# Performance work log

Hardware: AMD Instinct MI355X
Metric: run time of the kernel (lower is better)

The kernel has to match this reference:

```python
import jax, jax.numpy as jnp
import numpy as np

B, N, DOP, DM, H = 8, 2048, 256, 256, 256  # batch, n_ops==n_machines, dims


def setup_inputs() -> dict:
    key = jax.random.key(0)
    ks = jax.random.split(key, 21)
    s = 0.02
    inp = {
        "operation_features": jax.random.normal(ks[0], (B, N, DOP), jnp.float32),
        "machine_features": jax.random.normal(ks[1], (B, N, DM), jnp.float32),
        "type_match_mask": jax.random.bernoulli(ks[2], 0.3, (B, N, N)).astype(jnp.float32),
        "same_type_mask": jax.random.bernoulli(ks[3], 0.3, (B, N, N)).astype(jnp.float32),
        "oma_q_w": jax.random.normal(ks[4], (H, DM), jnp.float32) * s,
        "oma_q_b": jnp.zeros((H,), jnp.float32),
        "oma_kv_w": jax.random.normal(ks[5], (2 * H, DOP), jnp.float32) * s,
        "oma_kv_b": jnp.zeros((2 * H,), jnp.float32),
        "oma_s_w": jax.random.normal(ks[6], (1, 2 * H), jnp.float32) * s,
        "oma_s_b": jnp.zeros((1,), jnp.float32),
        "oma_o_w": jax.random.normal(ks[7], (DM, H), jnp.float32) * s,
        "oma_o_b": jnp.zeros((DM,), jnp.float32),
        "sa_w_w": jax.random.normal(ks[8], (3 * H, DM), jnp.float32) * s,
        "sa_w_b": jnp.zeros((3 * H,), jnp.float32),
        "sa_s_w": jax.random.normal(ks[9], (1, 2 * H), jnp.float32) * s,
        "sa_s_b": jnp.zeros((1,), jnp.float32),
        "sa_o_w": jax.random.normal(ks[10], (DM, H), jnp.float32) * s,
        "sa_o_b": jnp.zeros((DM,), jnp.float32),
        "mix_w": jax.random.normal(ks[11], (DM, 2 * DM), jnp.float32) * s,
        "mix_b": jnp.zeros((DM,), jnp.float32),
    }
    return inp


def reference(operation_features, machine_features, type_match_mask, same_type_mask,
              oma_q_w, oma_q_b, oma_kv_w, oma_kv_b, oma_s_w, oma_s_b, oma_o_w, oma_o_b,
              sa_w_w, sa_w_b, sa_s_w, sa_s_b, sa_o_w, sa_o_b, mix_w, mix_b):
    # --- OperationMachineAttention ---
    q = machine_features @ oma_q_w.T + oma_q_b            # (B,M,H)
    kv = operation_features @ oma_kv_w.T + oma_kv_b       # (B,C,2H)
    k, v = jnp.split(kv, 2, axis=-1)
    # Linear(cat([q,k])) == q @ W[:, :H].T + k @ W[:, H:].T + b (additive-score factorization)
    sq = jnp.einsum('bmh,h->bm', q, oma_s_w[0, :H])
    sk = jnp.einsum('bch,h->bc', k, oma_s_w[0, H:])
    scores = jax.nn.leaky_relu(sq[:, :, None] + sk[:, None, :] + oma_s_b[0])  # (B,M,C)
    p = jax.nn.softmax(scores * type_match_mask, axis=-1)
    wf = jnp.einsum('bmc,bch->bmh', p, v)
    operation_machine = wf @ oma_o_w.T + oma_o_b           # (B,M,DM)

    # --- SelfAttention over machines ---
    w3 = machine_features @ sa_w_w.T + sa_w_b              # (B,C,3H)
    q2, k2, v2 = jnp.split(w3, 3, axis=-1)
    sq2 = jnp.einsum('bih,h->bi', q2, sa_s_w[0, :H])
    sk2 = jnp.einsum('bjh,h->bj', k2, sa_s_w[0, H:])
    s2 = jax.nn.leaky_relu(sq2[:, :, None] + sk2[:, None, :] + sa_s_b[0])  # (B,C,C)
    p2 = jax.nn.softmax(s2 * same_type_mask, axis=-1)
    machine_machine = jnp.einsum('bij,bjh->bih', p2, v2) @ sa_o_w.T + sa_o_b  # (B,C,DM)

    # --- mix ---
    mixed = jnp.concatenate([operation_machine, machine_machine], axis=-1)
    return mixed @ mix_w.T + mix_b                          # (B,N,DM)
```

## Files before the change

### kernel.cpp

```cpp
#include <hip/hip_runtime.h>
#include <stdint.h>
#include <stddef.h>

#define B_ 8
#define N_ 2048
#define C_ 2048
#define D_ 256
#define H_ 256

typedef __bf16 bf16x8 __attribute__((ext_vector_type(8)));
typedef __bf16 bf16x4 __attribute__((ext_vector_type(4)));
typedef float f32x4 __attribute__((ext_vector_type(4)));

#define MFMA16(a, b, c) __builtin_amdgcn_mfma_f32_16x16x32_bf16((a), (b), (c), 0, 0, 0)

__global__ __launch_bounds__(256) void k0a_partial(
    const float* __restrict__ oma_q_w, const float* __restrict__ oma_kv_w,
    const float* __restrict__ sa_w_w,
    const float* __restrict__ oma_s_w, const float* __restrict__ sa_s_w,
    float* __restrict__ partial)
{
    int d = threadIdx.x;
    int vec = blockIdx.x >> 3, hc = blockIdx.x & 7;
    int h0 = hc * 32;
    const float* Wb; const float* sv;
    if (vec == 0)      { Wb = oma_q_w  + h0 * 256;         sv = oma_s_w + h0; }
    else if (vec == 1) { Wb = oma_kv_w + h0 * 256;         sv = oma_s_w + 256 + h0; }
    else if (vec == 2) { Wb = sa_w_w   + h0 * 256;         sv = sa_s_w + h0; }
    else               { Wb = sa_w_w   + (256 + h0) * 256; sv = sa_s_w + 256 + h0; }
    float a = 0.f;
    #pragma unroll 8
    for (int h = 0; h < 32; ++h) a += Wb[h * 256 + d] * sv[h];
    partial[blockIdx.x * 256 + d] = a;
}

__global__ __launch_bounds__(256) void k0b_reduce(
    const float* __restrict__ partial,
    const float* __restrict__ oma_q_b, const float* __restrict__ oma_kv_b,
    const float* __restrict__ oma_s_w, const float* __restrict__ oma_s_b,
    const float* __restrict__ sa_w_b, const float* __restrict__ sa_s_w,
    const float* __restrict__ sa_s_b,
    float* __restrict__ wq_v, float* __restrict__ wk_v,
    float* __restrict__ wq2_v, float* __restrict__ wk2_v,
    float* __restrict__ sb)
{
    int d = threadIdx.x;
    float a0 = 0.f, a1 = 0.f, a2 = 0.f, a3 = 0.f;
    #pragma unroll
    for (int hc = 0; hc < 8; ++hc) {
        a0 += partial[(0 * 8 + hc) * 256 + d];
        a1 += partial[(1 * 8 + hc) * 256 + d];
        a2 += partial[(2 * 8 + hc) * 256 + d];
        a3 += partial[(3 * 8 + hc) * 256 + d];
    }
    wq_v[d] = a0; wk_v[d] = a1; wq2_v[d] = a2; wk2_v[d] = a3;

    int h = d;
    float p1 = oma_q_b[h] * oma_s_w[h] + oma_kv_b[h] * oma_s_w[256 + h];
    float p2 = sa_w_b[h] * sa_s_w[h] + sa_w_b[256 + h] * sa_s_w[256 + h];
    for (int o = 32; o; o >>= 1) { p1 += __shfl_xor(p1, o); p2 += __shfl_xor(p2, o); }
    __shared__ float redA[4], redB[4];
    int wv = threadIdx.x >> 6;
    if ((threadIdx.x & 63) == 0) { redA[wv] = p1; redB[wv] = p2; }
    __syncthreads();
    if (threadIdx.x == 0) {
        sb[0] = redA[0] + redA[1] + redA[2] + redA[3] + oma_s_b[0];
        sb[1] = redB[0] + redB[1] + redB[2] + redB[3] + sa_s_b[0];
    }
}

__global__ __launch_bounds__(256) void k1_wcat(
    const float* __restrict__ mix_w, const float* __restrict__ mix_b,
    const float* __restrict__ oma_o_w, const float* __restrict__ oma_o_b,
    const float* __restrict__ sa_o_w, const float* __restrict__ sa_o_b,
    __bf16* __restrict__ Wcat, float* __restrict__ b_total)
{
    int d = blockIdx.x, h = threadIdx.x;
    const float* mwr = mix_w + d * 512;
    float w1 = 0.f, w2 = 0.f;
    for (int e = 0; e < 256; ++e) {
        w1 += mwr[e] * oma_o_w[e * 256 + h];
        w2 += mwr[256 + e] * sa_o_w[e * 256 + h];
    }
    Wcat[d * 512 + h] = (__bf16)w1;
    Wcat[d * 512 + 256 + h] = (__bf16)w2;

    float pb = mwr[h] * oma_o_b[h] + mwr[256 + h] * sa_o_b[h];
    for (int o = 32; o; o >>= 1) pb += __shfl_xor(pb, o);
    __shared__ float red[4];
    if ((h & 63) == 0) red[h >> 6] = pb;
    __syncthreads();
    if (h == 0) b_total[d] = mix_b[d] + red[0] + red[1] + red[2] + red[3];
}

__global__ __launch_bounds__(256) void k2_scores(
    const float* __restrict__ op, const float* __restrict__ mach,
    const float* __restrict__ wq_v, const float* __restrict__ wk_v,
    const float* __restrict__ wq2_v, const float* __restrict__ wk2_v,
    const float* __restrict__ sb,
    float* __restrict__ sqp, float* __restrict__ skv,
    float* __restrict__ sq2p, float* __restrict__ sk2v)
{
    int t = threadIdx.x, lane = t & 63, wv = t >> 6;
    size_t n = (size_t)blockIdx.x * 4 + wv;
    const float4 mf = *(const float4*)(mach + n * 256 + lane * 4);
    const float4 of = *(const float4*)(op + n * 256 + lane * 4);
    const float4 q4 = *(const float4*)(wq_v + lane * 4);
    const float4 k4 = *(const float4*)(wk_v + lane * 4);
    const float4 q24 = *(const float4*)(wq2_v + lane * 4);
    const float4 k24 = *(const float4*)(wk2_v + lane * 4);
    float s1 = mf.x * q4.x + mf.y * q4.y + mf.z * q4.z + mf.w * q4.w;
    float s2 = of.x * k4.x + of.y * k4.y + of.z * k4.z + of.w * k4.w;
    float s3 = mf.x * q24.x + mf.y * q24.y + mf.z * q24.z + mf.w * q24.w;
    float s4 = mf.x * k24.x + mf.y * k24.y + mf.z * k24.z + mf.w * k24.w;
    for (int o = 32; o; o >>= 1) {
        s1 += __shfl_xor(s1, o); s2 += __shfl_xor(s2, o);
        s3 += __shfl_xor(s3, o); s4 += __shfl_xor(s4, o);
    }
    if (lane == 0) {
        sqp[n] = s1 + sb[0]; skv[n] = s2;
        sq2p[n] = s3 + sb[1]; sk2v[n] = s4;
    }
}

__global__ __launch_bounds__(256, 2) void k3_vgemm(
    const float* __restrict__ op, const float* __restrict__ mach,
    const float* __restrict__ oma_kv_w, const float* __restrict__ sa_w_w,
    __bf16* __restrict__ vt)
{
    __shared__ __attribute__((aligned(16))) __bf16 As[64][72];
    __shared__ __attribute__((aligned(16))) __bf16 Bs[64][72];
    int t = threadIdx.x;
    int bid = blockIdx.x;
    int which = bid >> 10;
    int r = bid & 1023;
    int b = r >> 7;
    int ht = (r >> 5) & 3;
    int ct = r & 31;

    const float* Aglob = (which ? (sa_w_w + 512 * 256) : (oma_kv_w + 256 * 256)) + ht * 64 * 256;
    const float* Bglob = (which ? mach : op) + ((size_t)b * N_ + ct * 64) * 256;

    int lane = t & 63, wv = t >> 6;
    int l15 = lane & 15, qo = (lane >> 4) * 8;
    int rr = t >> 4;
    int dd = (t & 15) * 4;

    f32x4 acc[4] = {};

    for (int d0 = 0; d0 < 256; d0 += 64) {
        #pragma unroll
        for (int p = 0; p < 4; ++p) {
            float4 av = *(const float4*)(Aglob + (size_t)(p * 16 + rr) * 256 + d0 + dd);
            float4 bv = *(const float4*)(Bglob + (size_t)(p * 16 + rr) * 256 + d0 + dd);
            bf16x4 a4, b4;
            a4[0] = (__bf16)av.x; a4[1] = (__bf16)av.y; a4[2] = (__bf16)av.z; a4[3] = (__bf16)av.w;
            b4[0] = (__bf16)bv.x; b4[1] = (__bf16)bv.y; b4[2] = (__bf16)bv.z; b4[3] = (__bf16)bv.w;
            *(bf16x4*)&As[p * 16 + rr][dd] = a4;
            *(bf16x4*)&Bs[p * 16 + rr][dd] = b4;
        }
        __syncthreads();
        #pragma unroll
        for (int kb = 0; kb < 2; ++kb) {
            bf16x8 bfr = *(const bf16x8*)&Bs[16 * wv + l15][kb * 32 + qo];
            #pragma unroll
            for (int rt = 0; rt < 4; ++rt) {
                bf16x8 afr = *(const bf16x8*)&As[16 * rt + l15][kb * 32 + qo];
                acc[rt] = MFMA16(afr, bfr, acc[rt]);
            }
        }
        __syncthreads();
    }
    #pragma unroll
    for (int rt = 0; rt < 4; ++rt)
        #pragma unroll
        for (int j = 0; j < 4; ++j)
            As[16 * rt + (lane >> 4) * 4 + j][16 * wv + l15] = (__bf16)acc[rt][j];
    __syncthreads();
    int hh = t >> 2, cb = (t & 3) * 16;
    __bf16* orow = vt + (((size_t)(which * 8 + b)) * 256 + ht * 64 + hh) * 2048 + ct * 64 + cb;
    *(bf16x8*)(orow) = *(const bf16x8*)&As[hh][cb];
    *(bf16x8*)(orow + 8) = *(const bf16x8*)&As[hh][cb + 8];
}

__device__ __forceinline__ f32x4 ntload4f(const float* p) {
    return __builtin_nontemporal_load(reinterpret_cast<const f32x4*>(p));
}

__global__ __launch_bounds__(256, 4) void k4_attn(
    const float* __restrict__ tmask, const float* __restrict__ smask,
    const float* __restrict__ sqp, const float* __restrict__ skv,
    const float* __restrict__ sq2p, const float* __restrict__ sk2v,
    const __bf16* __restrict__ vt,
    __bf16* __restrict__ wfcat)
{
    __shared__ __attribute__((aligned(16))) __bf16 smem[32 * 264];
    __shared__ float rowsum[32];
    __bf16* eA0 = smem;
    __bf16* eA1 = smem + 32 * 72;

    int t = threadIdx.x;
    int bid = blockIdx.x;
    int wg = (bid & 7) * 128 + (bid >> 3);
    int which = wg >> 9;
    int r = wg & 511;
    int b = r >> 6;
    int m0 = (r & 63) * 32;

    const float* mask = (which ? smask : tmask) + ((size_t)b * N_ + m0) * C_;
    const float* sqrow = (which ? sq2p : sqp) + b * N_ + m0;
    const float* skrow = (which ? sk2v : skv) + b * N_;
    const __bf16* vbase = vt + ((size_t)(which * 8 + b)) * 256 * 2048;

    int lane = t & 63, wv = t >> 6;
    int l15 = lane & 15, qo = (lane >> 4) * 8;
    int mrow = t >> 3;
    int cq8 = (t & 7) * 8;

    const __bf16* vptr = vbase + (size_t)(64 * wv + l15) * 2048 + qo;
    const float* mrowp = mask + (size_t)mrow * C_ + cq8;

    float sqv = sqrow[mrow];
    float psum = 0.f;
    f32x4 acc[2][4] = {};

    bf16x8 bfr[4][2];
    float mkA[8], skA[8], mkB[8], skB[8];

    auto load_ms = [&](int c0, float* mk, float* sk) {
        f32x4 a = ntload4f(mrowp + c0);
        f32x4 bq = ntload4f(mrowp + c0 + 4);
        f32x4 s0 = *(const f32x4*)(skrow + c0 + cq8);
        f32x4 s1 = *(const f32x4*)(skrow + c0 + cq8 + 4);
        #pragma unroll
        for (int i = 0; i < 4; ++i) {
            mk[i] = a[i]; mk[4 + i] = bq[i];
            sk[i] = s0[i]; sk[4 + i] = s1[i];
        }
    };
    auto load_bfr = [&](int c0) {
        #pragma unroll
        for (int ct = 0; ct < 4; ++ct)
            #pragma unroll
            for (int kb = 0; kb < 2; ++kb)
                bfr[ct][kb] = *(const bf16x8*)(vptr + (size_t)ct * 16 * 2048 + c0 + kb * 32);
    };
    auto compute_e = [&](const float* mk, const float* sk, __bf16* eb) {
        bf16x8 ev;
        #pragma unroll
        for (int i = 0; i < 8; ++i) {
            float s = sqv + sk[i];
            s = s > 0.f ? s : 0.01f * s;
            float e = __expf(s * mk[i]);
            psum += e;
            ev[i] = (__bf16)e;
        }
        *(bf16x8*)&eb[mrow * 72 + cq8] = ev;
    };
    auto do_mfma = [&](const __bf16* eb) {
        #pragma unroll
        for (int kb = 0; kb < 2; ++kb) {
            bf16x8 afr0 = *(const bf16x8*)&eb[l15 * 72 + kb * 32 + qo];
            bf16x8 afr1 = *(const bf16x8*)&eb[(16 + l15) * 72 + kb * 32 + qo];
            #pragma unroll
            for (int ct = 0; ct < 4; ++ct) {
                acc[0][ct] = MFMA16(afr0, bfr[ct][kb], acc[0][ct]);
                acc[1][ct] = MFMA16(afr1, bfr[ct][kb], acc[1][ct]);
            }
        }
    };

    load_ms(0, mkA, skA);
    load_ms(64, mkB, skB);
    load_bfr(0);

    #pragma unroll 1
    for (int c0 = 0; c0 < C_; c0 += 128) {
        compute_e(mkA, skA, eA0);
        int cA = c0 + 128; if (cA >= C_) cA = 0;
        load_ms(cA, mkA, skA);
        asm volatile("s_waitcnt lgkmcnt(0)" ::: "memory");
        __builtin_amdgcn_s_barrier();
        do_mfma(eA0);
        load_bfr(c0 + 64);
        compute_e(mkB, skB, eA1);
        int cB = c0 + 192; if (cB >= C_) cB = 0;
        load_ms(cB, mkB, skB);
        asm volatile("s_waitcnt lgkmcnt(0)" ::: "memory");
        __builtin_amdgcn_s_barrier();
        do_mfma(eA1);
        int cN = c0 + 128; if (cN >= C_) cN = 0;
        load_bfr(cN);
    }

    float rs = psum;
    rs += __shfl_xor(rs, 1);
    rs += __shfl_xor(rs, 2);
    rs += __shfl_xor(rs, 4);
    if ((t & 7) == 0) rowsum[mrow] = rs;
    __syncthreads();

    __bf16* obuf = smem;
    #pragma unroll
    for (int rt = 0; rt < 2; ++rt) {
        #pragma unroll
        for (int j = 0; j < 4; ++j) {
            int m = 16 * rt + (lane >> 4) * 4 + j;
            float inv = __builtin_amdgcn_rcpf(rowsum[m]);
            #pragma unroll
            for (int ct = 0; ct < 4; ++ct)
                obuf[m * 264 + 64 * wv + 16 * ct + l15] = (__bf16)(acc[rt][ct][j] * inv);
        }
    }
    __syncthreads();
    int m = t >> 3, cb = (t & 7) * 32;
    __bf16* wrow = wfcat + ((size_t)(b * N_ + m0 + m)) * 512 + which * 256 + cb;
    #pragma unroll
    for (int k = 0; k < 4; ++k)
        *(bf16x8*)(wrow + k * 8) = *(const bf16x8*)&obuf[m * 264 + cb + k * 8];
}

__global__ __launch_bounds__(256, 2) void k5_out(
    const __bf16* __restrict__ wfcat, const __bf16* __restrict__ Wcat,
    const float* __restrict__ b_total, float* __restrict__ out)
{
    __shared__ __attribute__((aligned(16))) __bf16 As[32][72];
    __shared__ __attribute__((aligned(16))) __bf16 Bs[256][72];
    __shared__ float bias[256];
    int t = threadIdx.x;
    int n0 = blockIdx.x * 32;
    int lane = t & 63, wv = t >> 6, l15 = lane & 15, qo = (lane >> 4) * 8;
    bias[t] = b_total[t];
    int ar = t >> 3;
    int ac = (t & 7) * 8;
    f32x4 acc[2][4] = {};

    for (int k0 = 0; k0 < 512; k0 += 64) {
        *(bf16x8*)&As[ar][ac] =
            *(const bf16x8*)(wfcat + (size_t)(n0 + ar) * 512 + k0 + ac);
        #pragma unroll
        for (int p = 0; p < 8; ++p)
            *(bf16x8*)&Bs[p * 32 + ar][ac] =
                *(const bf16x8*)(Wcat + (size_t)(p * 32 + ar) * 512 + k0 + ac);
        __syncthreads();
        #pragma unroll
        for (int kb = 0; kb < 2; ++kb) {
            bf16x8 afr[2];
            #pragma unroll
            for (int rt = 0; rt < 2; ++rt)
                afr[rt] = *(const bf16x8*)&As[16 * rt + l15][kb * 32 + qo];
            #pragma unroll
            for (int ct = 0; ct < 4; ++ct) {
                bf16x8 bfr = *(const bf16x8*)&Bs[64 * wv + 16 * ct + l15][kb * 32 + qo];
                #pragma unroll
                for (int rt = 0; rt < 2; ++rt)
                    acc[rt][ct] = MFMA16(afr[rt], bfr, acc[rt][ct]);
            }
        }
        __syncthreads();
    }
    #pragma unroll
    for (int rt = 0; rt < 2; ++rt) {
        #pragma unroll
        for (int ct = 0; ct < 4; ++ct) {
            int d = 64 * wv + 16 * ct + l15;
            float bv = bias[d];
            #pragma unroll
            for (int j = 0; j < 4; ++j) {
                int m = 16 * rt + (lane >> 4) * 4 + j;
                out[(size_t)(n0 + m) * 256 + d] = acc[rt][ct][j] + bv;
            }
        }
    }
}

extern "C" void kernel_launch(void* const* d_in, const int* in_sizes, int n_in,
                              void* d_out, int out_size, void* d_ws, size_t ws_size,
                              hipStream_t stream)
{
    const float* op_feat  = (const float*)d_in[0];
    const float* mach_feat= (const float*)d_in[1];
    const float* tmask    = (const float*)d_in[2];
    const float* smask    = (const float*)d_in[3];
    const float* oma_q_w  = (const float*)d_in[4];
    const float* oma_q_b  = (const float*)d_in[5];
    const float* oma_kv_w = (const float*)d_in[6];
    const float* oma_kv_b = (const float*)d_in[7];
    const float* oma_s_w  = (const float*)d_in[8];
    const float* oma_s_b  = (const float*)d_in[9];
    const float* oma_o_w  = (const float*)d_in[10];
    const float* oma_o_b  = (const float*)d_in[11];
    const float* sa_w_w   = (const float*)d_in[12];
    const float* sa_w_b   = (const float*)d_in[13];
    const float* sa_s_w   = (const float*)d_in[14];
    const float* sa_s_b   = (const float*)d_in[15];
    const float* sa_o_w   = (const float*)d_in[16];
    const float* sa_o_b   = (const float*)d_in[17];
    const float* mix_w    = (const float*)d_in[18];
    const float* mix_b    = (const float*)d_in[19];

    char* ws = (char*)d_ws;
    float* wq_v   = (float*)(ws + 0);
    float* wk_v   = (float*)(ws + 1024);
    float* wq2_v  = (float*)(ws + 2048);
    float* wk2_v  = (float*)(ws + 3072);
    float* sb     = (float*)(ws + 4096);
    float* btot   = (float*)(ws + 4352);
    float* sqp    = (float*)(ws + 8192);
    float* skv    = (float*)(ws + 73728);
    float* sq2p   = (float*)(ws + 139264);
    float* sk2v   = (float*)(ws + 204800);
    __bf16* Wcat  = (__bf16*)(ws + 270336);
    __bf16* vt    = (__bf16*)(ws + 532480);
    __bf16* wfcat = (__bf16*)(ws + 17309696);
    float* outp   = (float*)d_out;

    float* partial = (float*)(ws + 532480);

    k0a_partial<<<32, 256, 0, stream>>>(oma_q_w, oma_kv_w, sa_w_w,
                                        oma_s_w, sa_s_w, partial);
    k0b_reduce<<<1, 256, 0, stream>>>(partial, oma_q_b, oma_kv_b, oma_s_w, oma_s_b,
                                      sa_w_b, sa_s_w, sa_s_b,
                                      wq_v, wk_v, wq2_v, wk2_v, sb);
    k1_wcat<<<256, 256, 0, stream>>>(mix_w, mix_b, oma_o_w, oma_o_b,
                                     sa_o_w, sa_o_b, Wcat, btot);
    k2_scores<<<4096, 256, 0, stream>>>(op_feat, mach_feat, wq_v, wk_v, wq2_v, wk2_v,
                                        sb, sqp, skv, sq2p, sk2v);
    k3_vgemm<<<2048, 256, 0, stream>>>(op_feat, mach_feat, oma_kv_w, sa_w_w, vt);
    k4_attn<<<1024, 256, 0, stream>>>(tmask, smask, sqp, skv, sq2p, sk2v, vt, wfcat);
    k5_out<<<512, 256, 0, stream>>>(wfcat, Wcat, btot, outp);
}
```

Before: 475.5 us.

## Double k4_attn row tile to 64 rows and double-buffer V fragments

Each attention workgroup now handles 64 query rows instead of 32, so every V fragment loaded from global memory feeds four row tiles of MFMAs instead of two. This halves V traffic per output row, and the grid shrinks from 1024 to 512 blocks. V fragments are now double-buffered in registers (vA/vB) and prefetched alongside the mask and score loads. The cost is a larger accumulator and register footprint, with launch bounds lowered to 2 waves per SIMD, so occupancy and latency hiding drop and there are fewer blocks to spread across CUs.

Result: faster. 450.0 us (-5.4%).

```diff
diff --git a/kernel.cpp b/kernel.cpp
--- a/kernel.cpp
+++ b/kernel.cpp
@@ -187,25 +187,25 @@
     return __builtin_nontemporal_load(reinterpret_cast<const f32x4*>(p));
 }
 
-__global__ __launch_bounds__(256, 4) void k4_attn(
+__global__ __launch_bounds__(256, 2) void k4_attn(
     const float* __restrict__ tmask, const float* __restrict__ smask,
     const float* __restrict__ sqp, const float* __restrict__ skv,
     const float* __restrict__ sq2p, const float* __restrict__ sk2v,
     const __bf16* __restrict__ vt,
     __bf16* __restrict__ wfcat)
 {
-    __shared__ __attribute__((aligned(16))) __bf16 smem[32 * 264];
-    __shared__ float rowsum[32];
+    __shared__ __attribute__((aligned(16))) __bf16 smem[64 * 264];
+    __shared__ float rowsum[64];
     __bf16* eA0 = smem;
-    __bf16* eA1 = smem + 32 * 72;
+    __bf16* eA1 = smem + 64 * 72;
 
     int t = threadIdx.x;
     int bid = blockIdx.x;
-    int wg = (bid & 7) * 128 + (bid >> 3);
-    int which = wg >> 9;
-    int r = wg & 511;
-    int b = r >> 6;
-    int m0 = (r & 63) * 32;
+    int wg = (bid & 7) * 64 + (bid >> 3);
+    int which = wg >> 8;
+    int r = wg & 255;
+    int b = r >> 5;
+    int m0 = (r & 31) * 64;
 
     const float* mask = (which ? smask : tmask) + ((size_t)b * N_ + m0) * C_;
     const float* sqrow = (which ? sq2p : sqp) + b * N_ + m0;
@@ -214,95 +214,95 @@
 
     int lane = t & 63, wv = t >> 6;
     int l15 = lane & 15, qo = (lane >> 4) * 8;
-    int mrow = t >> 3;
-    int cq8 = (t & 7) * 8;
+    int mrow = t >> 2;
+    int cq16 = (t & 3) * 16;
 
     const __bf16* vptr = vbase + (size_t)(64 * wv + l15) * 2048 + qo;
-    const float* mrowp = mask + (size_t)mrow * C_ + cq8;
+    const float* mrowp = mask + (size_t)mrow * C_ + cq16;
+    const float* skp = skrow + cq16;
 
     float sqv = sqrow[mrow];
     float psum = 0.f;
-    f32x4 acc[2][4] = {};
-
-    bf16x8 bfr[4][2];
-    float mkA[8], skA[8], mkB[8], skB[8];
-
-    auto load_ms = [&](int c0, float* mk, float* sk) {
-        f32x4 a = ntload4f(mrowp + c0);
-        f32x4 bq = ntload4f(mrowp + c0 + 4);
-        f32x4 s0 = *(const f32x4*)(skrow + c0 + cq8);
-        f32x4 s1 = *(const f32x4*)(skrow + c0 + cq8 + 4);
-        #pragma unroll
-        for (int i = 0; i < 4; ++i) {
-            mk[i] = a[i]; mk[4 + i] = bq[i];
-            sk[i] = s0[i]; sk[4 + i] = s1[i];
-        }
+    f32x4 acc[4][4] = {};
+
+    bf16x8 vA[8], vB[8];
+    f32x4 mkA[4], mkB[4], skA[4], skB[4];
+
+    auto load_v = [&](bf16x8* v, int c0) {
+        #pragma unroll
+        for (int ct = 0; ct < 4; ++ct)
+            #pragma unroll
+            for (int kb = 0; kb < 2; ++kb)
+                v[ct * 2 + kb] = *(const bf16x8*)(vptr + (size_t)ct * 16 * 2048 + c0 + kb * 32);
     };
-    auto load_bfr = [&](int c0) {
-        #pragma unroll
-        for (int ct = 0; ct < 4; ++ct)
-            #pragma unroll
-            for (int kb = 0; kb < 2; ++kb)
-                bfr[ct][kb] = *(const bf16x8*)(vptr + (size_t)ct * 16 * 2048 + c0 + kb * 32);
+    auto load_sk = [&](f32x4* sk, int c0) {
+        #pragma unroll
+        for (int i = 0; i < 4; ++i) sk[i] = *(const f32x4*)(skp + c0 + 4 * i);
     };
-    auto compute_e = [&](const float* mk, const float* sk, __bf16* eb) {
-        bf16x8 ev;
-        #pragma unroll
-        for (int i = 0; i < 8; ++i) {
-            float s = sqv + sk[i];
+    auto load_mk = [&](f32x4* mk, int c0) {
+        #pragma unroll
+        for (int i = 0; i < 4; ++i) mk[i] = ntload4f(mrowp + c0 + 4 * i);
+    };
+    auto compute_e = [&](const f32x4* mk, const f32x4* sk, __bf16* eb) {
+        bf16x8 e0, e1;
+        #pragma unroll
+        for (int i = 0; i < 16; ++i) {
+            float s = sqv + sk[i >> 2][i & 3];
             s = s > 0.f ? s : 0.01f * s;
-            float e = __expf(s * mk[i]);
+            float e = __expf(s * mk[i >> 2][i & 3]);
             psum += e;
-            ev[i] = (__bf16)e;
-        }
-        *(bf16x8*)&eb[mrow * 72 + cq8] = ev;
+            if (i < 8) e0[i] = (__bf16)e; else e1[i - 8] = (__bf16)e;
+        }
+        *(bf16x8*)&eb[mrow * 72 + cq16] = e0;
+        *(bf16x8*)&eb[mrow * 72 + cq16 + 8] = e1;
     };
-    auto do_mfma = [&](const __bf16* eb) {
+    auto do_mfma = [&](const __bf16* eb, const bf16x8* v) {
         #pragma unroll
         for (int kb = 0; kb < 2; ++kb) {
-            bf16x8 afr0 = *(const bf16x8*)&eb[l15 * 72 + kb * 32 + qo];
-            bf16x8 afr1 = *(const bf16x8*)&eb[(16 + l15) * 72 + kb * 32 + qo];
-            #pragma unroll
-            for (int ct = 0; ct < 4; ++ct) {
-                acc[0][ct] = MFMA16(afr0, bfr[ct][kb], acc[0][ct]);
-                acc[1][ct] = MFMA16(afr1, bfr[ct][kb], acc[1][ct]);
-            }
+            bf16x8 afr[4];
+            #pragma unroll
+            for (int rt = 0; rt < 4; ++rt)
+                afr[rt] = *(const bf16x8*)&eb[(16 * rt + l15) * 72 + kb * 32 + qo];
+            #pragma unroll
+            for (int ct = 0; ct < 4; ++ct)
+                #pragma unroll
+                for (int rt = 0; rt < 4; ++rt)
+                    acc[rt][ct] = MFMA16(afr[rt], v[ct * 2 + kb], acc[rt][ct]);
         }
     };
 
-    load_ms(0, mkA, skA);
-    load_ms(64, mkB, skB);
-    load_bfr(0);
+    load_v(vA, 0);
+    load_sk(skA, 0);
+    load_mk(mkA, 0);
+    load_mk(mkB, 64);
 
     #pragma unroll 1
     for (int c0 = 0; c0 < C_; c0 += 128) {
         compute_e(mkA, skA, eA0);
-        int cA = c0 + 128; if (cA >= C_) cA = 0;
-        load_ms(cA, mkA, skA);
+        load_v(vB, (c0 + 64) & (C_ - 1));
+        load_sk(skB, (c0 + 64) & (C_ - 1));
+        load_mk(mkA, (c0 + 128) & (C_ - 1));
         asm volatile("s_waitcnt lgkmcnt(0)" ::: "memory");
         __builtin_amdgcn_s_barrier();
-        do_mfma(eA0);
-        load_bfr(c0 + 64);
+        do_mfma(eA0, vA);
         compute_e(mkB, skB, eA1);
-        int cB = c0 + 192; if (cB >= C_) cB = 0;
-        load_ms(cB, mkB, skB);
+        load_v(vA, (c0 + 128) & (C_ - 1));
+        load_sk(skA, (c0 + 128) & (C_ - 1));
+        load_mk(mkB, (c0 + 192) & (C_ - 1));
         asm volatile("s_waitcnt lgkmcnt(0)" ::: "memory");
         __builtin_amdgcn_s_barrier();
-        do_mfma(eA1);
-        int cN = c0 + 128; if (cN >= C_) cN = 0;
-        load_bfr(cN);
+        do_mfma(eA1, vB);
     }
 
     float rs = psum;
     rs += __shfl_xor(rs, 1);
     rs += __shfl_xor(rs, 2);
-    rs += __shfl_xor(rs, 4);
-    if ((t & 7) == 0) rowsum[mrow] = rs;
+    if ((t & 3) == 0) rowsum[mrow] = rs;
     __syncthreads();
 
     __bf16* obuf = smem;
     #pragma unroll
-    for (int rt = 0; rt < 2; ++rt) {
+    for (int rt = 0; rt < 4; ++rt) {
         #pragma unroll
         for (int j = 0; j < 4; ++j) {
             int m = 16 * rt + (lane >> 4) * 4 + j;
@@ -313,10 +313,10 @@
         }
     }
     __syncthreads();
-    int m = t >> 3, cb = (t & 7) * 32;
+    int m = t >> 2, cb = (t & 3) * 64;
     __bf16* wrow = wfcat + ((size_t)(b * N_ + m0 + m)) * 512 + which * 256 + cb;
     #pragma unroll
-    for (int k = 0; k < 4; ++k)
+    for (int k = 0; k < 8; ++k)
         *(bf16x8*)(wrow + k * 8) = *(const bf16x8*)&obuf[m * 264 + cb + k * 8];
 }
 
@@ -427,6 +427,6 @@
     k2_scores<<<4096, 256, 0, stream>>>(op_feat, mach_feat, wq_v, wk_v, wq2_v, wk2_v,
                                         sb, sqp, skv, sq2p, sk2v);
     k3_vgemm<<<2048, 256, 0, stream>>>(op_feat, mach_feat, oma_kv_w, sa_w_w, vt);
-    k4_attn<<<1024, 256, 0, stream>>>(tmask, smask, sqp, skv, sq2p, sk2v, vt, wfcat);
+    k4_attn<<<512, 256, 0, stream>>>(tmask, smask, sqp, skv, sq2p, sk2v, vt, wfcat);
     k5_out<<<512, 256, 0, stream>>>(wfcat, Wcat, btot, outp);
 }
```
